# Performance work log

Measured on AMD Instinct MI355X. Metric: run time of the kernel, lower is better.

The kernel has to match this reference:

```python
import math
import jax, jax.numpy as jnp
import numpy as np

INPUT_DIM = 512
HIDDEN_DIM = 512
BATCH = 8
SEQ_LEN = 4096


def _xavier(key, shape):
    fan_out, fan_in = shape
    limit = math.sqrt(6.0 / (fan_in + fan_out))
    return jax.random.uniform(key, shape, jnp.float32, -limit, limit)


def setup_inputs() -> dict:
    key = jax.random.key(0)
    kx, kA, kB, kC, kD, kWg = jax.random.split(key, 6)
    return {
        "x": jax.random.normal(kx, (BATCH, SEQ_LEN, INPUT_DIM), jnp.float32),
        "A": jax.random.uniform(kA, (HIDDEN_DIM,), jnp.float32, 0.8, 0.95),
        "B": _xavier(kB, (HIDDEN_DIM, INPUT_DIM)),
        "C": _xavier(kC, (HIDDEN_DIM, HIDDEN_DIM)),
        "D": _xavier(kD, (HIDDEN_DIM, INPUT_DIM)),
        "Wg": _xavier(kWg, (HIDDEN_DIM, INPUT_DIM)),
        "bias_h": jnp.zeros((HIDDEN_DIM,), jnp.float32),
        "bias_y": jnp.zeros((HIDDEN_DIM,), jnp.float32),
    }


def reference(x, A, B, C, D, Wg, bias_h, bias_y):
    # x: (b, t, i). Eval mode: dropout is identity.
    hidden_dim = A.shape[0]
    # Precompute all input-dependent per-step terms as batched GEMMs.
    g = jnp.clip(jax.nn.sigmoid(jnp.einsum('bti,hi->bth', x, Wg)), 0.05, 0.95)
    xB = jnp.einsum('bti,hi->bth', x, B)
    # h_t = h_{t-1} + g_t*(A*h_{t-1} + xB_t + bias_h - h_{t-1})
    #     = (1 - g_t*(1 - A)) * h_{t-1} + g_t*(xB_t + bias_h)
    a_coef = 1.0 - g * (1.0 - A)          # (b, t, h)
    b_coef = g * (xB + bias_h)            # (b, t, h)

    def step(h, ab):
        a_t, b_t = ab
        h = a_t * h + b_t
        return h, h

    h0 = jnp.zeros((x.shape[0], hidden_dim), x.dtype)
    _, hs = jax.lax.scan(step, h0, (jnp.swapaxes(a_coef, 0, 1), jnp.swapaxes(b_coef, 0, 1)))
    hs = jnp.swapaxes(hs, 0, 1)           # (b, t, h)

    scale = 1.0 / math.sqrt(hidden_dim)
    y = (jnp.einsum('bth,oh->bto', hs, C) + jnp.einsum('bti,hi->bth', x, D) + bias_y) * scale
    return y
```

## Files before the change

### kernel.cpp

```cpp
#include <hip/hip_runtime.h>
#include <math.h>

#define MTOT 32768
#define KD 512
#define HD 512
#define NB 8
#define TS 4096
#define NCHUNK 64
#define TCHUNK 64

typedef __attribute__((ext_vector_type(8))) short bf16x8;
typedef __attribute__((ext_vector_type(4))) float f32x4;
typedef __attribute__((ext_vector_type(4))) unsigned short us4;

#define GLD16(gsrc, ldst) __builtin_amdgcn_global_load_lds( \
    (const __attribute__((address_space(1))) void*)(gsrc),   \
    (__attribute__((address_space(3))) void*)(ldst), 16, 0, 0)

__device__ __forceinline__ unsigned short f2bf(float f) {
    unsigned u = __float_as_uint(f);
    return (unsigned short)((u + 0x7FFFu + ((u >> 16) & 1u)) >> 16);
}

__global__ __launch_bounds__(256) void cast_x(const float* __restrict__ src,
                                              unsigned short* __restrict__ dst) {
    const int i = (blockIdx.x * 256 + threadIdx.x) * 4;
    float4 v = *(const float4*)(src + i);
    us4 o; o.x = f2bf(v.x); o.y = f2bf(v.y); o.z = f2bf(v.z); o.w = f2bf(v.w);
    *(us4*)(dst + i) = o;
}

__global__ __launch_bounds__(256) void cast_w(const float* __restrict__ B,
                                              const float* __restrict__ D,
                                              const float* __restrict__ G,
                                              const float* __restrict__ C,
                                              unsigned short* __restrict__ dst) {
    const float* srcs[4] = {B, D, G, C};
    const float* s = srcs[blockIdx.y];
    unsigned short* d = dst + (size_t)blockIdx.y * (HD * KD);
    const int i = (blockIdx.x * 256 + threadIdx.x) * 4;
    float4 v = *(const float4*)(s + i);
    us4 o; o.x = f2bf(v.x); o.y = f2bf(v.y); o.z = f2bf(v.z); o.w = f2bf(v.w);
    *(us4*)(d + i) = o;
}

__global__ __launch_bounds__(256, 2) void in_gemm_mfma(
    const short* __restrict__ xb, const short* __restrict__ wmat,
    const float* __restrict__ Avec, const float* __restrict__ bias_h,
    float* __restrict__ a_out, float* __restrict__ b_out, float* __restrict__ xd_out)
{
    __shared__ __align__(16) short Xs[128 * 64];
    __shared__ __align__(16) short Ws[3][64 * 64];
    const int tid = threadIdx.x;
    const int w = tid >> 6, l = tid & 63;
    const int m0 = blockIdx.x * 128;
    const int n0 = blockIdx.y * 64;
    const int wm = (w & 1) * 64;
    const int wn = (w >> 1) * 32;

    int xsrc[4], xdst[4];
    #pragma unroll
    for (int j = 0; j < 4; ++j) {
        const int s = (w * 4 + j) * 64 + l;
        const int r = s >> 3, g = (s & 7) ^ (r & 7);
        xsrc[j] = (m0 + r) * KD + g * 8;
        xdst[j] = (w * 4 + j) * 64 * 8;
    }
    int wsrc[2], wdst[2];
    #pragma unroll
    for (int j = 0; j < 2; ++j) {
        const int s = (w * 2 + j) * 64 + l;
        const int r = s >> 3, g = (s & 7) ^ (r & 7);
        wsrc[j] = (n0 + r) * KD + g * 8;
        wdst[j] = (w * 2 + j) * 64 * 8;
    }

    f32x4 acc[3][4][2];
    #pragma unroll
    for (int a = 0; a < 3; ++a)
        #pragma unroll
        for (int i = 0; i < 4; ++i)
            #pragma unroll
            for (int j = 0; j < 2; ++j) acc[a][i][j] = (f32x4)0.0f;

    for (int kk = 0; kk < KD; kk += 64) {
        __syncthreads();
        #pragma unroll
        for (int j = 0; j < 4; ++j) GLD16(xb + xsrc[j] + kk, Xs + xdst[j]);
        #pragma unroll
        for (int mat = 0; mat < 3; ++mat)
            #pragma unroll
            for (int j = 0; j < 2; ++j)
                GLD16(wmat + (size_t)mat * (HD * KD) + wsrc[j] + kk, &Ws[mat][wdst[j]]);
        __syncthreads();
        #pragma unroll
        for (int kc = 0; kc < 2; ++kc) {
            const int g = kc * 4 + (l >> 4);
            bf16x8 af[4];
            #pragma unroll
            for (int mt = 0; mt < 4; ++mt) {
                const int r = wm + mt * 16 + (l & 15);
                af[mt] = *(const bf16x8*)(Xs + r * 64 + ((g ^ (r & 7)) * 8));
            }
            #pragma unroll
            for (int mat = 0; mat < 3; ++mat) {
                #pragma unroll
                for (int nt = 0; nt < 2; ++nt) {
                    const int r = wn + nt * 16 + (l & 15);
                    bf16x8 bf = *(const bf16x8*)(&Ws[mat][r * 64 + ((g ^ (r & 7)) * 8)]);
                    #pragma unroll
                    for (int mt = 0; mt < 4; ++mt)
                        acc[mat][mt][nt] = __builtin_amdgcn_mfma_f32_16x16x32_bf16(
                            af[mt], bf, acc[mat][mt][nt], 0, 0, 0);
                }
            }
        }
    }

    #pragma unroll
    for (int nt = 0; nt < 2; ++nt) {
        const int n = n0 + wn + nt * 16 + (l & 15);
        const float An = Avec[n], bh = bias_h[n];
        #pragma unroll
        for (int mt = 0; mt < 4; ++mt) {
            #pragma unroll
            for (int r = 0; r < 4; ++r) {
                const int m = m0 + wm + mt * 16 + (l >> 4) * 4 + r;
                const size_t off = (size_t)m * HD + n;
                const float vB = acc[0][mt][nt][r];
                const float vD = acc[1][mt][nt][r];
                const float vG = acc[2][mt][nt][r];
                float g = 1.0f / (1.0f + expf(-vG));
                g = fminf(fmaxf(g, 0.05f), 0.95f);
                a_out[off]  = 1.0f - g * (1.0f - An);
                b_out[off]  = g * (vB + bh);
                xd_out[off] = vD;
            }
        }
    }
}

__global__ __launch_bounds__(256) void scan_pass1(
    const float* __restrict__ a_buf, const float* __restrict__ b_buf,
    float* __restrict__ chP, float* __restrict__ chS)
{
    const int g = blockIdx.x * blockDim.x + threadIdx.x;
    const int h = g & (HD - 1);
    const int rest = g >> 9;
    const int b = rest & (NB - 1);
    const int c = rest >> 3;
    size_t idx = ((size_t)(b * TS + c * TCHUNK)) * HD + h;
    float P = 1.0f, S = 0.0f;
    #pragma unroll 4
    for (int t = 0; t < TCHUNK; ++t) {
        const float av = a_buf[idx];
        const float bv = b_buf[idx];
        P *= av;
        S = fmaf(av, S, bv);
        idx += HD;
    }
    const int bh = b * HD + h;
    chP[(size_t)c * (NB * HD) + bh] = P;
    chS[(size_t)c * (NB * HD) + bh] = S;
}

__global__ __launch_bounds__(256) void scan_pass2(
    const float* __restrict__ chP, const float* __restrict__ chS,
    float* __restrict__ hin)
{
    const int bh = blockIdx.x * blockDim.x + threadIdx.x;
    float h = 0.0f;
    for (int c = 0; c < NCHUNK; ++c) {
        hin[(size_t)c * (NB * HD) + bh] = h;
        h = fmaf(chP[(size_t)c * (NB * HD) + bh], h, chS[(size_t)c * (NB * HD) + bh]);
    }
}

__global__ __launch_bounds__(256) void scan_pass3(
    const float* __restrict__ a_buf, const float* __restrict__ b_buf,
    const float* __restrict__ hin, unsigned short* __restrict__ hs_out)
{
    const int g = blockIdx.x * blockDim.x + threadIdx.x;
    const int h = g & (HD - 1);
    const int rest = g >> 9;
    const int b = rest & (NB - 1);
    const int c = rest >> 3;
    size_t idx = ((size_t)(b * TS + c * TCHUNK)) * HD + h;
    const int bh = b * HD + h;
    float hv = hin[(size_t)c * (NB * HD) + bh];
    #pragma unroll 4
    for (int t = 0; t < TCHUNK; ++t) {
        hv = fmaf(a_buf[idx], hv, b_buf[idx]);
        hs_out[idx] = f2bf(hv);
        idx += HD;
    }
}

__global__ __launch_bounds__(256, 2) void out_gemm_mfma(
    const short* __restrict__ hs, const short* __restrict__ Cb,
    const float* __restrict__ bias_y, float* __restrict__ y )
{
    __shared__ __align__(16) short Hs[128 * 64];
    __shared__ __align__(16) short Cs[128 * 64];
    const int tid = threadIdx.x;
    const int w = tid >> 6, l = tid & 63;
    const int m0 = blockIdx.x * 128;
    const int n0 = blockIdx.y * 128;
    const int wm = (w & 1) * 64;
    const int wn = (w >> 1) * 64;

    int src_h[4], src_c[4], dst_s[4];
    #pragma unroll
    for (int j = 0; j < 4; ++j) {
        const int s = (w * 4 + j) * 64 + l;
        const int r = s >> 3, g = (s & 7) ^ (r & 7);
        src_h[j] = (m0 + r) * HD + g * 8;
        src_c[j] = (n0 + r) * HD + g * 8;
        dst_s[j] = (w * 4 + j) * 64 * 8;
    }

    f32x4 acc[4][4];
    #pragma unroll
    for (int i = 0; i < 4; ++i)
        #pragma unroll
        for (int j = 0; j < 4; ++j) acc[i][j] = (f32x4)0.0f;

    for (int kk = 0; kk < HD; kk += 64) {
        __syncthreads();
        #pragma unroll
        for (int j = 0; j < 4; ++j) {
            GLD16(hs + src_h[j] + kk, Hs + dst_s[j]);
            GLD16(Cb + src_c[j] + kk, Cs + dst_s[j]);
        }
        __syncthreads();
        #pragma unroll
        for (int kc = 0; kc < 2; ++kc) {
            const int g = kc * 4 + (l >> 4);
            bf16x8 af[4], bf[4];
            #pragma unroll
            for (int t = 0; t < 4; ++t) {
                const int ra = wm + t * 16 + (l & 15);
                af[t] = *(const bf16x8*)(Hs + ra * 64 + ((g ^ (ra & 7)) * 8));
                const int rb = wn + t * 16 + (l & 15);
                bf[t] = *(const bf16x8*)(Cs + rb * 64 + ((g ^ (rb & 7)) * 8));
            }
            #pragma unroll
            for (int mt = 0; mt < 4; ++mt)
                #pragma unroll
                for (int nt = 0; nt < 4; ++nt)
                    acc[mt][nt] = __builtin_amdgcn_mfma_f32_16x16x32_bf16(
                        af[mt], bf[nt], acc[mt][nt], 0, 0, 0);
        }
    }

    const float scale = 0.04419417382415922f;
    #pragma unroll
    for (int nt = 0; nt < 4; ++nt) {
        const int n = n0 + wn + nt * 16 + (l & 15);
        const float by = bias_y[n];
        #pragma unroll
        for (int mt = 0; mt < 4; ++mt) {
            #pragma unroll
            for (int r = 0; r < 4; ++r) {
                const int m = m0 + wm + mt * 16 + (l >> 4) * 4 + r;
                const size_t off = (size_t)m * HD + n;
                y[off] = (acc[mt][nt][r] + y[off] + by) * scale;
            }
        }
    }
}

extern "C" void kernel_launch(void* const* d_in, const int* in_sizes, int n_in,
                              void* d_out, int out_size, void* d_ws, size_t ws_size,
                              hipStream_t stream) {
    const float* x      = (const float*)d_in[0];
    const float* Avec   = (const float*)d_in[1];
    const float* Bw     = (const float*)d_in[2];
    const float* Cw     = (const float*)d_in[3];
    const float* Dw     = (const float*)d_in[4];
    const float* Wg     = (const float*)d_in[5];
    const float* bias_h = (const float*)d_in[6];
    const float* bias_y = (const float*)d_in[7];
    float* y = (float*)d_out;

    float* a_buf = (float*)d_ws;
    float* b_buf = a_buf + (size_t)MTOT * HD;
    unsigned short* x16 = (unsigned short*)(b_buf + (size_t)MTOT * HD);
    unsigned short* w16 = x16 + (size_t)MTOT * HD;
    float* chP = (float*)(w16 + (size_t)4 * HD * KD);
    float* chS = chP + (size_t)NCHUNK * NB * HD;
    float* hin = chS + (size_t)NCHUNK * NB * HD;

    cast_x<<<MTOT * KD / 1024, 256, 0, stream>>>(x, x16);
    cast_w<<<dim3(HD * KD / 1024, 4), 256, 0, stream>>>(Bw, Dw, Wg, Cw, w16);

    in_gemm_mfma<<<dim3(MTOT / 128, HD / 64), 256, 0, stream>>>(
        (const short*)x16, (const short*)w16, Avec, bias_h, a_buf, b_buf, y);

    const int scan_threads = NB * HD * NCHUNK;
    scan_pass1<<<scan_threads / 256, 256, 0, stream>>>(a_buf, b_buf, chP, chS);
    scan_pass2<<<(NB * HD) / 256, 256, 0, stream>>>(chP, chS, hin);
    scan_pass3<<<scan_threads / 256, 256, 0, stream>>>(a_buf, b_buf, hin, x16);

    out_gemm_mfma<<<dim3(MTOT / 128, HD / 128), 256, 0, stream>>>(
        (const short*)x16, (const short*)(w16 + (size_t)3 * HD * KD), bias_y, y);
}
```

Baseline: 290.4 us.

## Fuse chunk-scan pass1 into input GEMM epilogue and pack coefficients as bf16

The input GEMM epilogue now computes per-64-step chunk products and sums with warp shuffles, so the separate scan_pass1 kernel and its full re-read of the a/b buffers go away. The a and b coefficients are stored as one packed bf16 pair per element, and the x·D term is stored as bf16 instead of fp32 into y. Together these cut intermediate memory traffic roughly in half. The cost is lower precision in the recurrence coefficients and the skip term, so errors can accumulate over the 4096-step scan.

```diff
diff --git a/kernel.cpp b/kernel.cpp
--- a/kernel.cpp
+++ b/kernel.cpp
@@ -20,6 +20,9 @@
 __device__ __forceinline__ unsigned short f2bf(float f) {
     unsigned u = __float_as_uint(f);
     return (unsigned short)((u + 0x7FFFu + ((u >> 16) & 1u)) >> 16);
+}
+__device__ __forceinline__ float bf2f(unsigned short u) {
+    return __uint_as_float(((unsigned)u) << 16);
 }
 
 __global__ __launch_bounds__(256) void cast_x(const float* __restrict__ src,
@@ -47,7 +50,8 @@
 __global__ __launch_bounds__(256, 2) void in_gemm_mfma(
     const short* __restrict__ xb, const short* __restrict__ wmat,
     const float* __restrict__ Avec, const float* __restrict__ bias_h,
-    float* __restrict__ a_out, float* __restrict__ b_out, float* __restrict__ xd_out)
+    unsigned* __restrict__ ab16, unsigned short* __restrict__ xd16,
+    float2* __restrict__ chPS)
 {
     __shared__ __align__(16) short Xs[128 * 64];
     __shared__ __align__(16) short Ws[3][64 * 64];
@@ -107,42 +111,81 @@
                 #pragma unroll
                 for (int nt = 0; nt < 2; ++nt) {
                     const int r = wn + nt * 16 + (l & 15);
-                    bf16x8 bf = *(const bf16x8*)(&Ws[mat][r * 64 + ((g ^ (r & 7)) * 8)]);
+                    bf16x8 bfv = *(const bf16x8*)(&Ws[mat][r * 64 + ((g ^ (r & 7)) * 8)]);
                     #pragma unroll
                     for (int mt = 0; mt < 4; ++mt)
                         acc[mat][mt][nt] = __builtin_amdgcn_mfma_f32_16x16x32_bf16(
-                            af[mt], bf, acc[mat][mt][nt], 0, 0, 0);
+                            af[mt], bfv, acc[mat][mt][nt], 0, 0, 0);
                 }
             }
         }
     }
 
+    const int q  = l >> 4;
+    const int cl = l & 15;
+    const int bidx   = m0 >> 12;
+    const int c_in_b = ((m0 & (TS - 1)) >> 6) + (w & 1);
     #pragma unroll
     for (int nt = 0; nt < 2; ++nt) {
-        const int n = n0 + wn + nt * 16 + (l & 15);
-        const float An = Avec[n], bh = bias_h[n];
+        const int n = n0 + wn + nt * 16 + cl;
+        const float An1 = 1.0f - Avec[n];
+        const float bh  = bias_h[n];
+        float Pc = 1.0f, Sc = 0.0f;
         #pragma unroll
         for (int mt = 0; mt < 4; ++mt) {
+            float Pl = 1.0f, Sl = 0.0f;
             #pragma unroll
             for (int r = 0; r < 4; ++r) {
-                const int m = m0 + wm + mt * 16 + (l >> 4) * 4 + r;
-                const size_t off = (size_t)m * HD + n;
                 const float vB = acc[0][mt][nt][r];
-                const float vD = acc[1][mt][nt][r];
                 const float vG = acc[2][mt][nt][r];
                 float g = 1.0f / (1.0f + expf(-vG));
                 g = fminf(fmaxf(g, 0.05f), 0.95f);
-                a_out[off]  = 1.0f - g * (1.0f - An);
-                b_out[off]  = g * (vB + bh);
-                xd_out[off] = vD;
-            }
-        }
-    }
-}
-
-__global__ __launch_bounds__(256) void scan_pass1(
-    const float* __restrict__ a_buf, const float* __restrict__ b_buf,
-    float* __restrict__ chP, float* __restrict__ chS)
+                const unsigned short su = f2bf(g * An1);
+                const unsigned short bu = f2bf(g * (vB + bh));
+                const float a  = 1.0f - bf2f(su);
+                const float bb = bf2f(bu);
+                const int m = m0 + wm + mt * 16 + q * 4 + r;
+                const size_t off = (size_t)m * HD + n;
+                ab16[off] = (unsigned)su | ((unsigned)bu << 16);
+                xd16[off] = f2bf(acc[1][mt][nt][r]);
+                Sl = fmaf(a, Sl, bb);
+                Pl *= a;
+            }
+            float Pm = 1.0f, Sm = 0.0f;
+            #pragma unroll
+            for (int k = 0; k < 4; ++k) {
+                const float Pk = __shfl(Pl, cl + 16 * k, 64);
+                const float Sk = __shfl(Sl, cl + 16 * k, 64);
+                Sm = fmaf(Pk, Sm, Sk);
+                Pm *= Pk;
+            }
+            Sc = fmaf(Pm, Sc, Sm);
+            Pc *= Pm;
+        }
+        if (q == 0) {
+            const size_t bh_i = (size_t)bidx * HD + n;
+            chPS[bh_i * NCHUNK + c_in_b] = make_float2(Pc, Sc);
+        }
+    }
+}
+
+__global__ __launch_bounds__(256) void scan_pass2(
+    const float2* __restrict__ chPS, float* __restrict__ hin)
+{
+    const int bh = blockIdx.x * blockDim.x + threadIdx.x;
+    const float2* p = chPS + (size_t)bh * NCHUNK;
+    float h = 0.0f;
+    #pragma unroll
+    for (int c = 0; c < NCHUNK; ++c) {
+        hin[(size_t)c * (NB * HD) + bh] = h;
+        const float2 ps = p[c];
+        h = fmaf(ps.x, h, ps.y);
+    }
+}
+
+__global__ __launch_bounds__(256) void scan_pass3(
+    const unsigned* __restrict__ ab, const float* __restrict__ hin,
+    unsigned short* __restrict__ hs_out)
 {
     const int g = blockIdx.x * blockDim.x + threadIdx.x;
     const int h = g & (HD - 1);
@@ -150,47 +193,13 @@
     const int b = rest & (NB - 1);
     const int c = rest >> 3;
     size_t idx = ((size_t)(b * TS + c * TCHUNK)) * HD + h;
-    float P = 1.0f, S = 0.0f;
+    float hv = hin[(size_t)c * (NB * HD) + b * HD + h];
     #pragma unroll 4
     for (int t = 0; t < TCHUNK; ++t) {
-        const float av = a_buf[idx];
-        const float bv = b_buf[idx];
-        P *= av;
-        S = fmaf(av, S, bv);
-        idx += HD;
-    }
-    const int bh = b * HD + h;
-    chP[(size_t)c * (NB * HD) + bh] = P;
-    chS[(size_t)c * (NB * HD) + bh] = S;
-}
-
-__global__ __launch_bounds__(256) void scan_pass2(
-    const float* __restrict__ chP, const float* __restrict__ chS,
-    float* __restrict__ hin)
-{
-    const int bh = blockIdx.x * blockDim.x + threadIdx.x;
-    float h = 0.0f;
-    for (int c = 0; c < NCHUNK; ++c) {
-        hin[(size_t)c * (NB * HD) + bh] = h;
-        h = fmaf(chP[(size_t)c * (NB * HD) + bh], h, chS[(size_t)c * (NB * HD) + bh]);
-    }
-}
-
-__global__ __launch_bounds__(256) void scan_pass3(
-    const float* __restrict__ a_buf, const float* __restrict__ b_buf,
-    const float* __restrict__ hin, unsigned short* __restrict__ hs_out)
-{
-    const int g = blockIdx.x * blockDim.x + threadIdx.x;
-    const int h = g & (HD - 1);
-    const int rest = g >> 9;
-    const int b = rest & (NB - 1);
-    const int c = rest >> 3;
-    size_t idx = ((size_t)(b * TS + c * TCHUNK)) * HD + h;
-    const int bh = b * HD + h;
-    float hv = hin[(size_t)c * (NB * HD) + bh];
-    #pragma unroll 4
-    for (int t = 0; t < TCHUNK; ++t) {
-        hv = fmaf(a_buf[idx], hv, b_buf[idx]);
+        const unsigned v = ab[idx];
+        const float a  = 1.0f - bf2f((unsigned short)(v & 0xFFFFu));
+        const float bb = bf2f((unsigned short)(v >> 16));
+        hv = fmaf(a, hv, bb);
         hs_out[idx] = f2bf(hv);
         idx += HD;
     }
@@ -198,7 +207,8 @@
 
 __global__ __launch_bounds__(256, 2) void out_gemm_mfma(
     const short* __restrict__ hs, const short* __restrict__ Cb,
-    const float* __restrict__ bias_y, float* __restrict__ y )
+    const unsigned short* __restrict__ xd16,
+    const float* __restrict__ bias_y, float* __restrict__ y)
 {
     __shared__ __align__(16) short Hs[128 * 64];
     __shared__ __align__(16) short Cs[128 * 64];
@@ -236,20 +246,20 @@
         #pragma unroll
         for (int kc = 0; kc < 2; ++kc) {
             const int g = kc * 4 + (l >> 4);
-            bf16x8 af[4], bf[4];
+            bf16x8 af[4], bfv[4];
             #pragma unroll
             for (int t = 0; t < 4; ++t) {
                 const int ra = wm + t * 16 + (l & 15);
                 af[t] = *(const bf16x8*)(Hs + ra * 64 + ((g ^ (ra & 7)) * 8));
                 const int rb = wn + t * 16 + (l & 15);
-                bf[t] = *(const bf16x8*)(Cs + rb * 64 + ((g ^ (rb & 7)) * 8));
+                bfv[t] = *(const bf16x8*)(Cs + rb * 64 + ((g ^ (rb & 7)) * 8));
             }
             #pragma unroll
             for (int mt = 0; mt < 4; ++mt)
                 #pragma unroll
                 for (int nt = 0; nt < 4; ++nt)
                     acc[mt][nt] = __builtin_amdgcn_mfma_f32_16x16x32_bf16(
-                        af[mt], bf[nt], acc[mt][nt], 0, 0, 0);
+                        af[mt], bfv[nt], acc[mt][nt], 0, 0, 0);
         }
     }
 
@@ -264,7 +274,7 @@
             for (int r = 0; r < 4; ++r) {
                 const int m = m0 + wm + mt * 16 + (l >> 4) * 4 + r;
                 const size_t off = (size_t)m * HD + n;
-                y[off] = (acc[mt][nt][r] + y[off] + by) * scale;
+                y[off] = (acc[mt][nt][r] + bf2f(xd16[off]) + by) * scale;
             }
         }
     }
@@ -283,25 +293,22 @@
     const float* bias_y = (const float*)d_in[7];
     float* y = (float*)d_out;
 
-    float* a_buf = (float*)d_ws;
-    float* b_buf = a_buf + (size_t)MTOT * HD;
-    unsigned short* x16 = (unsigned short*)(b_buf + (size_t)MTOT * HD);
-    unsigned short* w16 = x16 + (size_t)MTOT * HD;
-    float* chP = (float*)(w16 + (size_t)4 * HD * KD);
-    float* chS = chP + (size_t)NCHUNK * NB * HD;
-    float* hin = chS + (size_t)NCHUNK * NB * HD;
+    unsigned* ab16       = (unsigned*)d_ws;
+    unsigned short* xd16 = (unsigned short*)(ab16 + (size_t)MTOT * HD);
+    unsigned short* x16  = xd16 + (size_t)MTOT * HD;
+    unsigned short* w16  = x16 + (size_t)MTOT * HD;
+    float2* chPS = (float2*)(w16 + (size_t)4 * HD * KD);
+    float* hin   = (float*)(chPS + (size_t)NB * HD * NCHUNK);
 
     cast_x<<<MTOT * KD / 1024, 256, 0, stream>>>(x, x16);
     cast_w<<<dim3(HD * KD / 1024, 4), 256, 0, stream>>>(Bw, Dw, Wg, Cw, w16);
 
     in_gemm_mfma<<<dim3(MTOT / 128, HD / 64), 256, 0, stream>>>(
-        (const short*)x16, (const short*)w16, Avec, bias_h, a_buf, b_buf, y);
-
-    const int scan_threads = NB * HD * NCHUNK;
-    scan_pass1<<<scan_threads / 256, 256, 0, stream>>>(a_buf, b_buf, chP, chS);
-    scan_pass2<<<(NB * HD) / 256, 256, 0, stream>>>(chP, chS, hin);
-    scan_pass3<<<scan_threads / 256, 256, 0, stream>>>(a_buf, b_buf, hin, x16);
+        (const short*)x16, (const short*)w16, Avec, bias_h, ab16, xd16, chPS);
+
+    scan_pass2<<<(NB * HD) / 256, 256, 0, stream>>>(chPS, hin);
+    scan_pass3<<<(NB * HD * NCHUNK) / 256, 256, 0, stream>>>(ab16, hin, x16);
 
     out_gemm_mfma<<<dim3(MTOT / 128, HD / 128), 256, 0, stream>>>(
-        (const short*)x16, (const short*)(w16 + (size_t)3 * HD * KD), bias_y, y);
-}
+        (const short*)x16, (const short*)(w16 + (size_t)3 * HD * KD), xd16, bias_y, y);
+}
```

After: 272.6 us. -6.1%, faster.
